# Performance work log

Hardware: AMD Instinct MI355X
Metric: run time of the kernel (lower is better)

The kernel has to match this reference:

```python
import jax, jax.numpy as jnp
import numpy as np
from jax import lax

B = 16           # graphs per batch
N_PER = 4096     # points per graph (equal-sized graphs)
C_IN = 32        # in_channels
RATIO = 0.25
MAX_NBR = 32     # max_num_neighbors in radius()


def _xavier(key, fan_in, fan_out):
    lim = np.sqrt(6.0 / (fan_in + fan_out)).astype(np.float32)
    return jax.random.uniform(key, (fan_in, fan_out), jnp.float32, -lim, lim)


def setup_inputs() -> dict:
    key = jax.random.key(0)
    ks = jax.random.split(key, 16)
    x = jax.random.normal(ks[0], (B * N_PER, C_IN), jnp.float32)
    pos = jax.random.uniform(ks[1], (B * N_PER, 3), jnp.float32) * 20.0
    batch = jnp.repeat(jnp.arange(B, dtype=jnp.int64), N_PER)
    p = {
        'x': x, 'pos': pos, 'batch': batch,
        'scaler_mean': jnp.zeros((1, C_IN), jnp.float32),
        'scaler_std': jnp.ones((1, C_IN), jnp.float32),
        # SA1: Linear(32+3,64) -> Sigmoid -> Linear(64,128)
        'sa1_w1': _xavier(ks[2], C_IN + 3, 64), 'sa1_b1': jnp.zeros((64,), jnp.float32),
        'sa1_w2': _xavier(ks[3], 64, 128),      'sa1_b2': jnp.zeros((128,), jnp.float32),
        # SA2: Linear(128+3,128) -> Sigmoid -> Linear(128,256)
        'sa2_w1': _xavier(ks[4], 128 + 3, 128), 'sa2_b1': jnp.zeros((128,), jnp.float32),
        'sa2_w2': _xavier(ks[5], 128, 256),     'sa2_b2': jnp.zeros((256,), jnp.float32),
        # Global SA: Linear(256+3,256) -> Sigmoid -> Linear(256,512)
        'g_w1': _xavier(ks[6], 256 + 3, 256),   'g_b1': jnp.zeros((256,), jnp.float32),
        'g_w2': _xavier(ks[7], 256, 512),       'g_b2': jnp.zeros((512,), jnp.float32),
        # fc: Linear(512,256) -> Sigmoid -> Linear(256,128)
        'fc_w1': _xavier(ks[8], 512, 256),      'fc_b1': jnp.zeros((256,), jnp.float32),
        'fc_w2': _xavier(ks[9], 256, 128),      'fc_b2': jnp.zeros((128,), jnp.float32),
    }
    return p


def _fps(pos, k):
    # Farthest point sampling, deterministic start at index 0. pos: [B, n, 3] -> idx [B, k]
    pos = lax.stop_gradient(pos)
    d0 = jnp.sum((pos - pos[:, :1, :]) ** 2, -1)  # [B, n] dist^2 to start point

    def step(mind, _):
        nxt = jnp.argmax(mind, axis=1)                                  # [B]
        p = jnp.take_along_axis(pos, nxt[:, None, None], axis=1)        # [B,1,3]
        mind = jnp.minimum(mind, jnp.sum((pos - p) ** 2, -1))
        return mind, nxt

    _, rest = lax.scan(step, d0, None, length=k - 1)                    # [k-1, B]
    start = jnp.zeros((1, pos.shape[0]), rest.dtype)
    return jnp.concatenate([start, rest], 0).T                          # [B, k]


def _gather_nbr(v, nbr):
    # v: [B, n, C], nbr: [B, k, MAX_NBR] -> [B, k, MAX_NBR, C]
    return jax.vmap(lambda vb, nb: vb[nb])(v, nbr)


def _sa_module(x, pos, w1, b1, w2, b2, ratio, r):
    # PointNetConv (max aggregation) over a radius graph from FPS centers.
    Bb, n, _ = x.shape
    k = int(n * ratio)
    idx = _fps(pos, k)                                                  # [B, k]
    pos_dst = jnp.take_along_axis(pos, idx[:, :, None], axis=1)         # [B, k, 3]
    d2 = jnp.sum((pos_dst[:, :, None, :] - pos[:, None, :, :]) ** 2, -1)  # [B,k,n]
    masked = jnp.where(d2 <= r * r, d2, jnp.inf)
    negv, nbr = lax.top_k(-masked, MAX_NBR)                             # nearest <=32 within radius
    valid = jnp.isfinite(negv)                                          # [B,k,32]
    x_j = _gather_nbr(x, nbr)                                           # [B,k,32,C]
    rel = _gather_nbr(pos, nbr) - pos_dst[:, :, None, :]                # pos_j - pos_i
    feat = jnp.concatenate([x_j, rel], axis=-1)
    msg = jax.nn.sigmoid(feat @ w1 + b1) @ w2 + b2                      # [B,k,32,2h]
    msg = jnp.where(valid[..., None], msg, -jnp.inf)
    agg = jnp.max(msg, axis=2)                                          # max aggregation
    agg = jnp.where(jnp.isfinite(agg), agg, 0.0)  # (self is always a neighbor, defensive)
    return jax.nn.relu(agg), pos_dst


def reference(x, pos, batch, scaler_mean, scaler_std,
              sa1_w1, sa1_b1, sa1_w2, sa1_b2,
              sa2_w1, sa2_b1, sa2_w2, sa2_b2,
              g_w1, g_b1, g_w2, g_b2,
              fc_w1, fc_b1, fc_w2, fc_b2):
    x = (x - scaler_mean) / scaler_std
    xb = x.reshape(B, N_PER, -1)      # batch is sorted with N_PER points per graph
    pb = pos.reshape(B, N_PER, 3)
    xb, pb = _sa_module(xb, pb, sa1_w1, sa1_b1, sa1_w2, sa1_b2, RATIO, 2.0)
    xb, pb = _sa_module(xb, pb, sa2_w1, sa2_b1, sa2_w2, sa2_b2, RATIO, 4.0)
    # GlobalSAModule: relu(nn(cat[x, pos])) then global max pool
    h = jnp.concatenate([xb, pb], axis=-1)
    h = jax.nn.relu(jax.nn.sigmoid(h @ g_w1 + g_b1) @ g_w2 + g_b2)      # [B, 256, 512]
    g = jnp.max(h, axis=1)                                              # [B, 512]
    out = jax.nn.sigmoid(g @ fc_w1 + fc_b1) @ fc_w2 + fc_b2
    return jax.nn.relu(out)                                             # last_act='relu'
```

## Files before the change

### kernel.cpp

```cpp
#include <hip/hip_runtime.h>
#include <hip/hip_bf16.h>
#include <math.h>

namespace {

constexpr int NB   = 16;
constexpr int N1   = 4096;
constexpr int K1   = 1024;
constexpr int K2   = 256;
constexpr int MAXN = 32;
constexpr int RCAP = 448;

__device__ __forceinline__ float sigmoidf_(float x) {
  return 1.0f / (1.0f + __expf(-x));
}

__device__ __forceinline__ float readlane_f(float v, int l) {
  return __int_as_float(__builtin_amdgcn_readlane(__float_as_int(v), l));
}


#define FPS_DPP_STEP(CTRL)                                                     \
  {                                                                            \
    const unsigned olo =                                                       \
        (unsigned)__builtin_amdgcn_update_dpp(0, (int)lo, (CTRL), 0xF, 0xF, true); \
    const unsigned ohi =                                                       \
        (unsigned)__builtin_amdgcn_update_dpp(0, (int)hi, (CTRL), 0xF, 0xF, true); \
    const unsigned long long o = ((unsigned long long)ohi << 32) | olo;        \
    const unsigned long long cur = ((unsigned long long)hi << 32) | lo;        \
    if (o > cur) { lo = olo; hi = ohi; }                                       \
  }

template<int NPT>
__device__ __forceinline__ void fps_level(
    const float* __restrict__ sx, const float* __restrict__ sy,
    const float* __restrict__ sz, int k,
    float* __restrict__ selx, float* __restrict__ sely,
    float* __restrict__ selz,
    unsigned long long (*red)[4]) {
  const int t = threadIdx.x;
  const int lane = t & 63, wave = t >> 6;
  float px[NPT], py[NPT], pz[NPT], mind[NPT];
  unsigned niv[NPT];
  const float c0x = sx[0], c0y = sy[0], c0z = sz[0];
  unsigned long long best = 0;
#pragma unroll
  for (int i = 0; i < NPT; i++) {
    const int p = i * 256 + t;
    niv[i] = ~(unsigned)p;
    px[i] = sx[p]; py[i] = sy[p]; pz[i] = sz[p];
    const float dx = px[i] - c0x, dy = py[i] - c0y, dz = pz[i] - c0z;
    const float d2 = dx * dx + dy * dy + dz * dz;
    mind[i] = d2;
    const unsigned long long cand =
        ((unsigned long long)__float_as_uint(d2) << 32) | niv[i];
    if (cand > best) best = cand;
  }
  if (t == 0) { selx[0] = c0x; sely[0] = c0y; selz[0] = c0z; }
  for (int it = 1; it < k; it++) {
    unsigned lo = (unsigned)best, hi = (unsigned)(best >> 32);
    FPS_DPP_STEP(0x111)
    FPS_DPP_STEP(0x112)
    FPS_DPP_STEP(0x114)
    FPS_DPP_STEP(0x118)
    FPS_DPP_STEP(0x142)
    FPS_DPP_STEP(0x143)
    const int par = it & 1;
    if (lane == 63) red[par][wave] = ((unsigned long long)hi << 32) | lo;
    __syncthreads();
    const unsigned long long w0 = red[par][0], w1 = red[par][1];
    const unsigned long long w2 = red[par][2], w3 = red[par][3];
    const unsigned long long m01 = w0 > w1 ? w0 : w1;
    const unsigned long long m23 = w2 > w3 ? w2 : w3;
    const unsigned long long win = m01 > m23 ? m01 : m23;
    const int p = (int)(~(unsigned)win);
    const float nx = sx[p], ny = sy[p], nz = sz[p];
    if (t == 0) { selx[it] = nx; sely[it] = ny; selz[it] = nz; }
    best = 0;
#pragma unroll
    for (int i = 0; i < NPT; i++) {
      const float dx = px[i] - nx, dy = py[i] - ny, dz = pz[i] - nz;
      const float d2 = dx * dx + dy * dy + dz * dz;
      const float m = fminf(mind[i], d2);
      mind[i] = m;
      const unsigned long long cand =
          ((unsigned long long)__float_as_uint(m) << 32) | niv[i];
      if (cand > best) best = cand;
    }
  }
}

#undef FPS_DPP_STEP

__global__ __launch_bounds__(256) void fps_l1_kernel(
    const float* __restrict__ pos,
    float* __restrict__ pxg, float* __restrict__ pyg, float* __restrict__ pzg,
    float* __restrict__ d1x, float* __restrict__ d1y, float* __restrict__ d1z,
    unsigned int* __restrict__ gout) {
  __shared__ float sx[N1], sy[N1], sz[N1];
  __shared__ float s2x[K1], s2y[K1], s2z[K1];
  __shared__ __align__(16) unsigned long long red[2][4];
  const int b = blockIdx.x;
  const int t = threadIdx.x;
  gout[b * 512 + t] = 0u;
  gout[b * 512 + t + 256] = 0u;
  const float* pb = pos + (size_t)b * N1 * 3;
  for (int p = t; p < N1; p += 256) {
    sx[p] = pb[p * 3 + 0]; sy[p] = pb[p * 3 + 1]; sz[p] = pb[p * 3 + 2];
  }
  __syncthreads();
  fps_level<N1 / 256>(sx, sy, sz, K1, s2x, s2y, s2z, red);
  __syncthreads();
  for (int p = t; p < N1; p += 256) {
    pxg[(size_t)b * N1 + p] = sx[p];
    pyg[(size_t)b * N1 + p] = sy[p];
    pzg[(size_t)b * N1 + p] = sz[p];
  }
  for (int i = t; i < K1; i += 256) {
    d1x[(size_t)b * K1 + i] = s2x[i];
    d1y[(size_t)b * K1 + i] = s2y[i];
    d1z[(size_t)b * K1 + i] = s2z[i];
  }
}

struct RadSmem {
  float candd[4][RCAP];
  int   candi[4][RCAP];
};

__device__ __forceinline__ void radius_body(
    const float* __restrict__ ptsx, const float* __restrict__ ptsy,
    const float* __restrict__ ptsz, int N,
    const float* __restrict__ cxs, const float* __restrict__ cys,
    const float* __restrict__ czs, int K, int CSTR, float r2,
    int* __restrict__ nbr, int* __restrict__ cnt_out, RadSmem& sm, int rb) {
  const int t = threadIdx.x;
  const int lane = t & 63, wave = t >> 6;
  const int bpg = K / 4;
  const int b = rb / bpg;
  const int ci = (rb % bpg) * 4 + wave;
  const size_t pbase = (size_t)b * N;
  const size_t cbase = (size_t)b * CSTR + ci;
  const float cx = cxs[cbase], cy = cys[cbase], cz = czs[cbase];
  int total = 0;
  for (int base = 0; base < N; base += 64) {
    const int p = base + lane;
    const float dx = ptsx[pbase + p] - cx;
    const float dy = ptsy[pbase + p] - cy;
    const float dz = ptsz[pbase + p] - cz;
    const float d2 = dx * dx + dy * dy + dz * dz;
    const bool pred = d2 <= r2;
    const unsigned long long m = __ballot(pred);
    if (pred) {
      const int slot = total + __popcll(m & ((1ull << lane) - 1ull));
      if (slot < RCAP) { sm.candd[wave][slot] = d2; sm.candi[wave][slot] = p; }
    }
    total += __popcll(m);
  }
  if (total > RCAP) total = RCAP;
  int* nbp = nbr + ((size_t)b * K + ci) * MAXN;
  if (total <= MAXN) {
    if (lane < total) nbp[lane] = sm.candi[wave][lane];
  } else {
    for (int jj = 0; jj < MAXN; jj++) {
      float bvd = INFINITY; int bvi = 0x7fffffff; int bslot = 0;
      for (int s = lane; s < total; s += 64) {
        const float d = sm.candd[wave][s];
        const int i = sm.candi[wave][s];
        if (d < bvd || (d == bvd && i < bvi)) { bvd = d; bvi = i; bslot = s; }
      }
#pragma unroll
      for (int off = 32; off; off >>= 1) {
        const float od = __shfl_xor(bvd, off);
        const int   oi = __shfl_xor(bvi, off);
        const int   os = __shfl_xor(bslot, off);
        if (od < bvd || (od == bvd && oi < bvi)) { bvd = od; bvi = oi; bslot = os; }
      }
      if (lane == 0) { nbp[jj] = bvi; sm.candd[wave][bslot] = INFINITY; }
    }
  }
  if (lane == 0) cnt_out[(size_t)b * K + ci] = (total < MAXN) ? total : MAXN;
}

__global__ __launch_bounds__(256) void rad12_kernel(
    const float* __restrict__ pxg, const float* __restrict__ pyg,
    const float* __restrict__ pzg,
    const float* __restrict__ d1x, const float* __restrict__ d1y,
    const float* __restrict__ d1z,
    int* __restrict__ nbr1, int* __restrict__ cnt1,
    int* __restrict__ nbr2, int* __restrict__ cnt2) {
  constexpr int NR1 = NB * K1 / 4;
  __shared__ __align__(16) RadSmem r;
  if (blockIdx.x < (unsigned)NR1) {
    radius_body(pxg, pyg, pzg, N1, d1x, d1y, d1z, K1, K1, 4.0f,
                nbr1, cnt1, r, blockIdx.x);
  } else {
    radius_body(d1x, d1y, d1z, K1, d1x, d1y, d1z, K2, K1, 16.0f,
                nbr2, cnt2, r, blockIdx.x - NR1);
  }
}

template<int CIN_T, int H, int COUT, bool SCALE>
__device__ __forceinline__ void sa_conv_body(
    const float* __restrict__ xin,
    const float* __restrict__ ptsx, const float* __restrict__ ptsy,
    const float* __restrict__ ptsz,
    const float* __restrict__ cxs, const float* __restrict__ cys,
    const float* __restrict__ czs,
    const int* __restrict__ nbr, const int* __restrict__ cnt,
    const float* __restrict__ w1, const float* __restrict__ b1,
    const float* __restrict__ w2, const float* __restrict__ b2,
    const float* __restrict__ smean, const float* __restrict__ sstd,
    int N, int K, int CSTR, float* __restrict__ xout,
    float* part , int bk) {
  constexpr int FIN  = CIN_T + 3;
  constexpr int KREG = (FIN + 63) / 64;
  constexpr int HREG = H / 64;
  constexpr int CREG = COUT / 64;
  constexpr int RPW  = MAXN / 4;
  const int t = threadIdx.x, lane = t & 63, wave = t >> 6;
  const int b = bk / K;
  const int V = cnt[bk];
  float m[CREG];
#pragma unroll
  for (int ck = 0; ck < CREG; ck++) m[ck] = -INFINITY;
  if (V > wave * RPW) {
    const int* nb = nbr + (size_t)bk * MAXN;
    const size_t crow = (size_t)b * CSTR + (bk - b * K);
    const float ctrx = cxs[crow];
    const float ctry = cys[crow];
    const float ctrz = czs[crow];
    float sm = 0.0f, sd = 1.0f;
    if (SCALE && lane < CIN_T) { sm = smean[lane]; sd = sstd[lane]; }
    float fr[RPW][KREG];
#pragma unroll
    for (int r = 0; r < RPW; r++) {
      const int j = wave * RPW + r;
      const int p = (j < V) ? nb[j] : nb[0];
#pragma unroll
      for (int k2 = 0; k2 < KREG; k2++) {
        const int f = k2 * 64 + lane;
        float v = 0.0f;
        if (f < CIN_T) {
          v = xin[((size_t)b * N + p) * CIN_T + f];
          if constexpr (SCALE) v = (v - sm) / sd;
        } else if (f < FIN) {
          const int d = f - CIN_T;
          const float pv = (d == 0 ? ptsx : (d == 1 ? ptsy : ptsz))[(size_t)b * N + p];
          v = pv - (d == 0 ? ctrx : (d == 1 ? ctry : ctrz));
        }
        fr[r][k2] = v;
      }
    }
    float hh[RPW][HREG];
    {
      float acc[RPW][HREG];
#pragma unroll
      for (int r = 0; r < RPW; r++)
#pragma unroll
        for (int q = 0; q < HREG; q++) acc[r][q] = 0.0f;
#pragma unroll
      for (int k2 = 0; k2 < KREG; k2++) {
        const int lim = (FIN - k2 * 64) < 64 ? (FIN - k2 * 64) : 64;
        for (int fl = 0; fl < lim; fl++) {
          const int f = k2 * 64 + fl;
          float wv[HREG];
          if constexpr (HREG == 1) {
            wv[0] = w1[(size_t)f * H + lane];
          } else {
            const float2 w = *reinterpret_cast<const float2*>(
                &w1[(size_t)f * H + lane * 2]);
            wv[0] = w.x; wv[1] = w.y;
          }
#pragma unroll
          for (int r = 0; r < RPW; r++) {
            const float s = readlane_f(fr[r][k2], fl);
#pragma unroll
            for (int q = 0; q < HREG; q++) acc[r][q] = fmaf(s, wv[q], acc[r][q]);
          }
        }
      }
#pragma unroll
      for (int q = 0; q < HREG; q++) {
        const float bb = b1[lane * HREG + q];
#pragma unroll
        for (int r = 0; r < RPW; r++) hh[r][q] = sigmoidf_(acc[r][q] + bb);
      }
    }
    float acc2[RPW][CREG];
#pragma unroll
    for (int r = 0; r < RPW; r++)
#pragma unroll
      for (int q = 0; q < CREG; q++) acc2[r][q] = 0.0f;
    for (int hl = 0; hl < 64; hl++) {
#pragma unroll
      for (int q1 = 0; q1 < HREG; q1++) {
        const int h = hl * HREG + q1;
        float wv[CREG];
        if constexpr (CREG == 2) {
          const float2 w = *reinterpret_cast<const float2*>(
              &w2[(size_t)h * COUT + lane * 2]);
          wv[0] = w.x; wv[1] = w.y;
        } else {
          const float4 w = *reinterpret_cast<const float4*>(
              &w2[(size_t)h * COUT + lane * 4]);
          wv[0] = w.x; wv[1] = w.y; wv[2] = w.z; wv[3] = w.w;
        }
#pragma unroll
        for (int r = 0; r < RPW; r++) {
          const float s = readlane_f(hh[r][q1], hl);
#pragma unroll
          for (int q = 0; q < CREG; q++) acc2[r][q] = fmaf(s, wv[q], acc2[r][q]);
        }
      }
    }
#pragma unroll
    for (int r = 0; r < RPW; r++) {
      if (wave * RPW + r < V) {
#pragma unroll
        for (int q = 0; q < CREG; q++) m[q] = fmaxf(m[q], acc2[r][q]);
      }
    }
  }
#pragma unroll
  for (int q = 0; q < CREG; q++) part[wave * COUT + lane * CREG + q] = m[q];
  __syncthreads();
  if (t < COUT) {
    const float mm = fmaxf(fmaxf(part[0 * COUT + t], part[1 * COUT + t]),
                           fmaxf(part[2 * COUT + t], part[3 * COUT + t]));
    const float o = mm + b2[t];
    xout[(size_t)bk * COUT + t] = o > 0.0f ? o : 0.0f;
  }
}

__global__ __launch_bounds__(256) void conv1_kernel(
    const float* __restrict__ x,
    const float* __restrict__ pxg, const float* __restrict__ pyg,
    const float* __restrict__ pzg,
    const float* __restrict__ d1x, const float* __restrict__ d1y,
    const float* __restrict__ d1z,
    const int* __restrict__ nbr1, const int* __restrict__ cnt1,
    const float* __restrict__ s1w1, const float* __restrict__ s1b1,
    const float* __restrict__ s1w2, const float* __restrict__ s1b2,
    const float* __restrict__ smean, const float* __restrict__ sstd,
    float* __restrict__ x1) {
  __shared__ __align__(16) float part[4 * 128];
  sa_conv_body<32, 64, 128, true>(x, pxg, pyg, pzg, d1x, d1y, d1z,
                                  nbr1, cnt1, s1w1, s1b1, s1w2, s1b2,
                                  smean, sstd, N1, K1, K1, x1, part,
                                  blockIdx.x);
}

__global__ __launch_bounds__(256) void conv2_kernel(
    const float* __restrict__ x1,
    const float* __restrict__ d1x, const float* __restrict__ d1y,
    const float* __restrict__ d1z,
    const int* __restrict__ nbr2, const int* __restrict__ cnt2,
    const float* __restrict__ s2w1, const float* __restrict__ s2b1,
    const float* __restrict__ s2w2, const float* __restrict__ s2b2,
    float* __restrict__ x2) {
  __shared__ __align__(16) float part[4 * 256];
  sa_conv_body<128, 128, 256, false>(x1, d1x, d1y, d1z, d1x, d1y, d1z,
                                     nbr2, cnt2, s2w1, s2b1, s2w2, s2b2,
                                     nullptr, nullptr, K1, K2, K1, x2, part,
                                     blockIdx.x);
}

__global__ __launch_bounds__(256) void global_sa_kernel(
    const float* __restrict__ x2,
    const float* __restrict__ d1x, const float* __restrict__ d1y,
    const float* __restrict__ d1z,
    const float* __restrict__ gw1, const float* __restrict__ gb1,
    const float* __restrict__ gw2, const float* __restrict__ gb2,
    unsigned int* __restrict__ gout) {
  __shared__ float fin[4][259];
  __shared__ float s[4][256];
  const int t = threadIdx.x;
  const int blk = blockIdx.x;
  const int b = blk / 64;
  const int p0 = (blk % 64) * 4;
  for (int item = t; item < 4 * 259; item += 256) {
    const int p = item / 259, f = item - p * 259;
    float v;
    if (f < 256) {
      v = x2[((size_t)b * 256 + p0 + p) * 256 + f];
    } else {
      const int d = f - 256;
      v = (d == 0 ? d1x : (d == 1 ? d1y : d1z))[(size_t)b * K1 + p0 + p];
    }
    fin[p][f] = v;
  }
  __syncthreads();
  float acc[4] = {0.f, 0.f, 0.f, 0.f};
  for (int f = 0; f < 259; f++) {
    const float w = gw1[f * 256 + t];
#pragma unroll
    for (int p = 0; p < 4; p++) acc[p] = fmaf(fin[p][f], w, acc[p]);
  }
  const float bb = gb1[t];
#pragma unroll
  for (int p = 0; p < 4; p++) s[p][t] = sigmoidf_(acc[p] + bb);
  __syncthreads();
  float a0[4] = {0.f, 0.f, 0.f, 0.f}, a1[4] = {0.f, 0.f, 0.f, 0.f};
  for (int h = 0; h < 256; h++) {
    const float w0 = gw2[h * 512 + t];
    const float w1v = gw2[h * 512 + t + 256];
#pragma unroll
    for (int p = 0; p < 4; p++) {
      a0[p] = fmaf(s[p][h], w0, a0[p]);
      a1[p] = fmaf(s[p][h], w1v, a1[p]);
    }
  }
  const float b0 = gb2[t], b1v = gb2[t + 256];
  float m0 = 0.0f, m1 = 0.0f;
#pragma unroll
  for (int p = 0; p < 4; p++) {
    m0 = fmaxf(m0, fmaxf(a0[p] + b0, 0.0f));
    m1 = fmaxf(m1, fmaxf(a1[p] + b1v, 0.0f));
  }
  atomicMax(&gout[b * 512 + t], __float_as_uint(m0));
  atomicMax(&gout[b * 512 + t + 256], __float_as_uint(m1));
}

__global__ __launch_bounds__(256) void fc_kernel(
    const unsigned int* __restrict__ g,
    const float* __restrict__ fw1, const float* __restrict__ fb1,
    const float* __restrict__ fw2, const float* __restrict__ fb2,
    float* __restrict__ out) {
  __shared__ float gv[512];
  __shared__ float s[256];
  const int b = blockIdx.x, t = threadIdx.x;
  gv[t] = __uint_as_float(g[b * 512 + t]);
  gv[t + 256] = __uint_as_float(g[b * 512 + t + 256]);
  __syncthreads();
  float acc = 0.0f;
  for (int h = 0; h < 512; h++) acc = fmaf(gv[h], fw1[h * 256 + t], acc);
  s[t] = sigmoidf_(acc + fb1[t]);
  __syncthreads();
  if (t < 128) {
    float a2 = 0.0f;
    for (int h = 0; h < 256; h++) a2 = fmaf(s[h], fw2[h * 128 + t], a2);
    const float o = a2 + fb2[t];
    out[b * 128 + t] = o > 0.0f ? o : 0.0f;
  }
}

}

extern "C" void kernel_launch(void* const* d_in, const int* in_sizes, int n_in,
                              void* d_out, int out_size, void* d_ws, size_t ws_size,
                              hipStream_t stream) {
  (void)in_sizes; (void)n_in; (void)out_size; (void)ws_size;
  const float* x     = (const float*)d_in[0];
  const float* pos   = (const float*)d_in[1];
  const float* smean = (const float*)d_in[3];
  const float* sstd  = (const float*)d_in[4];
  const float* s1w1  = (const float*)d_in[5];
  const float* s1b1  = (const float*)d_in[6];
  const float* s1w2  = (const float*)d_in[7];
  const float* s1b2  = (const float*)d_in[8];
  const float* s2w1  = (const float*)d_in[9];
  const float* s2b1  = (const float*)d_in[10];
  const float* s2w2  = (const float*)d_in[11];
  const float* s2b2  = (const float*)d_in[12];
  const float* gw1   = (const float*)d_in[13];
  const float* gb1   = (const float*)d_in[14];
  const float* gw2   = (const float*)d_in[15];
  const float* gb2   = (const float*)d_in[16];
  const float* fw1   = (const float*)d_in[17];
  const float* fb1   = (const float*)d_in[18];
  const float* fw2   = (const float*)d_in[19];
  const float* fb2   = (const float*)d_in[20];

  char* ws = (char*)d_ws;
  size_t off = 0;
  auto take = [&](size_t bytes) -> char* {
    char* p = ws + off;
    off = (off + bytes + 255) & ~(size_t)255;
    return p;
  };
  float* pxg         = (float*)take((size_t)NB * N1 * 4);
  float* pyg         = (float*)take((size_t)NB * N1 * 4);
  float* pzg         = (float*)take((size_t)NB * N1 * 4);
  float* d1x         = (float*)take((size_t)NB * K1 * 4);
  float* d1y         = (float*)take((size_t)NB * K1 * 4);
  float* d1z         = (float*)take((size_t)NB * K1 * 4);
  int*   nbr1        = (int*)take((size_t)NB * K1 * MAXN * 4);
  int*   cnt1        = (int*)take((size_t)NB * K1 * 4);
  float* x1          = (float*)take((size_t)NB * K1 * 128 * 4);
  int*   nbr2        = (int*)take((size_t)NB * K2 * MAXN * 4);
  int*   cnt2        = (int*)take((size_t)NB * K2 * 4);
  float* x2          = (float*)take((size_t)NB * K2 * 256 * 4);
  unsigned int* gbuf = (unsigned int*)take((size_t)NB * 512 * 4);

  hipLaunchKernelGGL(fps_l1_kernel, dim3(NB), dim3(256), 0, stream,
                     pos, pxg, pyg, pzg, d1x, d1y, d1z, gbuf);
  hipLaunchKernelGGL(rad12_kernel, dim3(NB * K1 / 4 + NB * K2 / 4), dim3(256), 0, stream,
                     pxg, pyg, pzg, d1x, d1y, d1z, nbr1, cnt1, nbr2, cnt2);
  hipLaunchKernelGGL(conv1_kernel, dim3(NB * K1), dim3(256), 0, stream,
                     x, pxg, pyg, pzg, d1x, d1y, d1z, nbr1, cnt1,
                     s1w1, s1b1, s1w2, s1b2, smean, sstd, x1);
  hipLaunchKernelGGL(conv2_kernel, dim3(NB * K2), dim3(256), 0, stream,
                     x1, d1x, d1y, d1z, nbr2, cnt2,
                     s2w1, s2b1, s2w2, s2b2, x2);
  hipLaunchKernelGGL(global_sa_kernel, dim3(NB * 64), dim3(256), 0, stream,
                     x2, d1x, d1y, d1z, gw1, gb1, gw2, gb2, gbuf);
  hipLaunchKernelGGL(fc_kernel, dim3(NB), dim3(256), 0, stream,
                     gbuf, fw1, fb1, fw2, fb2, (float*)d_out);
}
```

Baseline: 1.150 ms.

## Overlap FPS with radius and conv1 in a persistent cooperative kernel

Replaces the separate FPS, radius and conv1 launches with one cooperative persistent kernel. Sixteen blocks run farthest-point sampling and publish progress through release-stored flags every four samples. The remaining blocks take work items from an atomic counter, spin until their centers are ready, then run the radius search and conv1 for four centers, keeping neighbor lists in LDS. The second-level radius search is also fused into the conv2 kernel, removing the global neighbor buffers and two launches. The trade-offs are spin-wait overhead, relying on the cooperative launch to make all 256 blocks co-resident, and subtle memory-ordering assumptions on the position writes.

```diff
diff --git a/kernel.cpp b/kernel.cpp
--- a/kernel.cpp
+++ b/kernel.cpp
@@ -32,12 +32,11 @@
   }
 
 template<int NPT>
-__device__ __forceinline__ void fps_level(
+__device__ __forceinline__ void fps_run(
     const float* __restrict__ sx, const float* __restrict__ sy,
     const float* __restrict__ sz, int k,
-    float* __restrict__ selx, float* __restrict__ sely,
-    float* __restrict__ selz,
-    unsigned long long (*red)[4]) {
+    float* __restrict__ dgx, float* __restrict__ dgy, float* __restrict__ dgz,
+    int* readyp, unsigned long long (*red)[4]) {
   const int t = threadIdx.x;
   const int lane = t & 63, wave = t >> 6;
   float px[NPT], py[NPT], pz[NPT], mind[NPT];
@@ -56,7 +55,7 @@
         ((unsigned long long)__float_as_uint(d2) << 32) | niv[i];
     if (cand > best) best = cand;
   }
-  if (t == 0) { selx[0] = c0x; sely[0] = c0y; selz[0] = c0z; }
+  if (t == 0) { dgx[0] = c0x; dgy[0] = c0y; dgz[0] = c0z; }
   for (int it = 1; it < k; it++) {
     unsigned lo = (unsigned)best, hi = (unsigned)(best >> 32);
     FPS_DPP_STEP(0x111)
@@ -75,7 +74,12 @@
     const unsigned long long win = m01 > m23 ? m01 : m23;
     const int p = (int)(~(unsigned)win);
     const float nx = sx[p], ny = sy[p], nz = sz[p];
-    if (t == 0) { selx[it] = nx; sely[it] = ny; selz[it] = nz; }
+    if (t == 0) {
+      dgx[it] = nx; dgy[it] = ny; dgz[it] = nz;
+      if ((it & 3) == 3)
+        __hip_atomic_store(readyp, it + 1, __ATOMIC_RELEASE,
+                           __HIP_MEMORY_SCOPE_AGENT);
+    }
     best = 0;
 #pragma unroll
     for (int i = 0; i < NPT; i++) {
@@ -88,66 +92,28 @@
       if (cand > best) best = cand;
     }
   }
+  if (t == 0)
+    __hip_atomic_store(readyp, k, __ATOMIC_RELEASE, __HIP_MEMORY_SCOPE_AGENT);
 }
 
 #undef FPS_DPP_STEP
-
-__global__ __launch_bounds__(256) void fps_l1_kernel(
-    const float* __restrict__ pos,
-    float* __restrict__ pxg, float* __restrict__ pyg, float* __restrict__ pzg,
-    float* __restrict__ d1x, float* __restrict__ d1y, float* __restrict__ d1z,
-    unsigned int* __restrict__ gout) {
-  __shared__ float sx[N1], sy[N1], sz[N1];
-  __shared__ float s2x[K1], s2y[K1], s2z[K1];
-  __shared__ __align__(16) unsigned long long red[2][4];
-  const int b = blockIdx.x;
-  const int t = threadIdx.x;
-  gout[b * 512 + t] = 0u;
-  gout[b * 512 + t + 256] = 0u;
-  const float* pb = pos + (size_t)b * N1 * 3;
-  for (int p = t; p < N1; p += 256) {
-    sx[p] = pb[p * 3 + 0]; sy[p] = pb[p * 3 + 1]; sz[p] = pb[p * 3 + 2];
-  }
-  __syncthreads();
-  fps_level<N1 / 256>(sx, sy, sz, K1, s2x, s2y, s2z, red);
-  __syncthreads();
-  for (int p = t; p < N1; p += 256) {
-    pxg[(size_t)b * N1 + p] = sx[p];
-    pyg[(size_t)b * N1 + p] = sy[p];
-    pzg[(size_t)b * N1 + p] = sz[p];
-  }
-  for (int i = t; i < K1; i += 256) {
-    d1x[(size_t)b * K1 + i] = s2x[i];
-    d1y[(size_t)b * K1 + i] = s2y[i];
-    d1z[(size_t)b * K1 + i] = s2z[i];
-  }
-}
 
 struct RadSmem {
   float candd[4][RCAP];
   int   candi[4][RCAP];
 };
 
-__device__ __forceinline__ void radius_body(
-    const float* __restrict__ ptsx, const float* __restrict__ ptsy,
-    const float* __restrict__ ptsz, int N,
-    const float* __restrict__ cxs, const float* __restrict__ cys,
-    const float* __restrict__ czs, int K, int CSTR, float r2,
-    int* __restrict__ nbr, int* __restrict__ cnt_out, RadSmem& sm, int rb) {
-  const int t = threadIdx.x;
-  const int lane = t & 63, wave = t >> 6;
-  const int bpg = K / 4;
-  const int b = rb / bpg;
-  const int ci = (rb % bpg) * 4 + wave;
-  const size_t pbase = (size_t)b * N;
-  const size_t cbase = (size_t)b * CSTR + ci;
-  const float cx = cxs[cbase], cy = cys[cbase], cz = czs[cbase];
+__device__ __forceinline__ void radius_lds(
+    const float* __restrict__ px, const float* __restrict__ py,
+    const float* __restrict__ pz, int N,
+    float cx, float cy, float cz, float r2,
+    RadSmem& sm, int* nb, int* cntp, int wave, int lane) {
   int total = 0;
   for (int base = 0; base < N; base += 64) {
     const int p = base + lane;
-    const float dx = ptsx[pbase + p] - cx;
-    const float dy = ptsy[pbase + p] - cy;
-    const float dz = ptsz[pbase + p] - cz;
+    const float dx = px[p] - cx;
+    const float dy = py[p] - cy;
+    const float dz = pz[p] - cz;
     const float d2 = dx * dx + dy * dy + dz * dz;
     const bool pred = d2 <= r2;
     const unsigned long long m = __ballot(pred);
@@ -158,9 +124,8 @@
     total += __popcll(m);
   }
   if (total > RCAP) total = RCAP;
-  int* nbp = nbr + ((size_t)b * K + ci) * MAXN;
   if (total <= MAXN) {
-    if (lane < total) nbp[lane] = sm.candi[wave][lane];
+    if (lane < total) nb[lane] = sm.candi[wave][lane];
   } else {
     for (int jj = 0; jj < MAXN; jj++) {
       float bvd = INFINITY; int bvi = 0x7fffffff; int bslot = 0;
@@ -176,60 +141,33 @@
         const int   os = __shfl_xor(bslot, off);
         if (od < bvd || (od == bvd && oi < bvi)) { bvd = od; bvi = oi; bslot = os; }
       }
-      if (lane == 0) { nbp[jj] = bvi; sm.candd[wave][bslot] = INFINITY; }
-    }
-  }
-  if (lane == 0) cnt_out[(size_t)b * K + ci] = (total < MAXN) ? total : MAXN;
-}
-
-__global__ __launch_bounds__(256) void rad12_kernel(
-    const float* __restrict__ pxg, const float* __restrict__ pyg,
-    const float* __restrict__ pzg,
-    const float* __restrict__ d1x, const float* __restrict__ d1y,
-    const float* __restrict__ d1z,
-    int* __restrict__ nbr1, int* __restrict__ cnt1,
-    int* __restrict__ nbr2, int* __restrict__ cnt2) {
-  constexpr int NR1 = NB * K1 / 4;
-  __shared__ __align__(16) RadSmem r;
-  if (blockIdx.x < (unsigned)NR1) {
-    radius_body(pxg, pyg, pzg, N1, d1x, d1y, d1z, K1, K1, 4.0f,
-                nbr1, cnt1, r, blockIdx.x);
-  } else {
-    radius_body(d1x, d1y, d1z, K1, d1x, d1y, d1z, K2, K1, 16.0f,
-                nbr2, cnt2, r, blockIdx.x - NR1);
-  }
+      if (lane == 0) { nb[jj] = bvi; sm.candd[wave][bslot] = INFINITY; }
+    }
+  }
+  if (lane == 0) *cntp = (total < MAXN) ? total : MAXN;
 }
 
 template<int CIN_T, int H, int COUT, bool SCALE>
-__device__ __forceinline__ void sa_conv_body(
+__device__ __forceinline__ void conv_center(
     const float* __restrict__ xin,
     const float* __restrict__ ptsx, const float* __restrict__ ptsy,
     const float* __restrict__ ptsz,
-    const float* __restrict__ cxs, const float* __restrict__ cys,
-    const float* __restrict__ czs,
-    const int* __restrict__ nbr, const int* __restrict__ cnt,
+    float ctrx, float ctry, float ctrz,
+    const int* nb, int V,
     const float* __restrict__ w1, const float* __restrict__ b1,
     const float* __restrict__ w2, const float* __restrict__ b2,
     const float* __restrict__ smean, const float* __restrict__ sstd,
-    int N, int K, int CSTR, float* __restrict__ xout,
-    float* part , int bk) {
+    float* __restrict__ outrow, float* part ) {
   constexpr int FIN  = CIN_T + 3;
   constexpr int KREG = (FIN + 63) / 64;
   constexpr int HREG = H / 64;
   constexpr int CREG = COUT / 64;
   constexpr int RPW  = MAXN / 4;
   const int t = threadIdx.x, lane = t & 63, wave = t >> 6;
-  const int b = bk / K;
-  const int V = cnt[bk];
   float m[CREG];
 #pragma unroll
   for (int ck = 0; ck < CREG; ck++) m[ck] = -INFINITY;
   if (V > wave * RPW) {
-    const int* nb = nbr + (size_t)bk * MAXN;
-    const size_t crow = (size_t)b * CSTR + (bk - b * K);
-    const float ctrx = cxs[crow];
-    const float ctry = cys[crow];
-    const float ctrz = czs[crow];
     float sm = 0.0f, sd = 1.0f;
     if (SCALE && lane < CIN_T) { sm = smean[lane]; sd = sstd[lane]; }
     float fr[RPW][KREG];
@@ -242,11 +180,11 @@
         const int f = k2 * 64 + lane;
         float v = 0.0f;
         if (f < CIN_T) {
-          v = xin[((size_t)b * N + p) * CIN_T + f];
+          v = xin[(size_t)p * CIN_T + f];
           if constexpr (SCALE) v = (v - sm) / sd;
         } else if (f < FIN) {
           const int d = f - CIN_T;
-          const float pv = (d == 0 ? ptsx : (d == 1 ? ptsy : ptsz))[(size_t)b * N + p];
+          const float pv = (d == 0 ? ptsx : (d == 1 ? ptsy : ptsz))[p];
           v = pv - (d == 0 ? ctrx : (d == 1 ? ctry : ctrz));
         }
         fr[r][k2] = v;
@@ -329,41 +267,109 @@
     const float mm = fmaxf(fmaxf(part[0 * COUT + t], part[1 * COUT + t]),
                            fmaxf(part[2 * COUT + t], part[3 * COUT + t]));
     const float o = mm + b2[t];
-    xout[(size_t)bk * COUT + t] = o > 0.0f ? o : 0.0f;
-  }
-}
-
-__global__ __launch_bounds__(256) void conv1_kernel(
-    const float* __restrict__ x,
-    const float* __restrict__ pxg, const float* __restrict__ pyg,
-    const float* __restrict__ pzg,
-    const float* __restrict__ d1x, const float* __restrict__ d1y,
-    const float* __restrict__ d1z,
-    const int* __restrict__ nbr1, const int* __restrict__ cnt1,
+    outrow[t] = o > 0.0f ? o : 0.0f;
+  }
+}
+
+__global__ __launch_bounds__(256) void phase1_kernel(
+    const float* __restrict__ pos, const float* __restrict__ x,
+    const float* __restrict__ smean, const float* __restrict__ sstd,
     const float* __restrict__ s1w1, const float* __restrict__ s1b1,
     const float* __restrict__ s1w2, const float* __restrict__ s1b2,
-    const float* __restrict__ smean, const float* __restrict__ sstd,
-    float* __restrict__ x1) {
-  __shared__ __align__(16) float part[4 * 128];
-  sa_conv_body<32, 64, 128, true>(x, pxg, pyg, pzg, d1x, d1y, d1z,
-                                  nbr1, cnt1, s1w1, s1b1, s1w2, s1b2,
-                                  smean, sstd, N1, K1, K1, x1, part,
-                                  blockIdx.x);
-}
-
-__global__ __launch_bounds__(256) void conv2_kernel(
+    float* __restrict__ pxg, float* __restrict__ pyg, float* __restrict__ pzg,
+    float* __restrict__ d1x, float* __restrict__ d1y, float* __restrict__ d1z,
+    float* __restrict__ x1, unsigned int* __restrict__ gout,
+    int* __restrict__ ctrl) {
+  __shared__ __align__(16) char smem[49152];
+  __shared__ __align__(16) unsigned long long red[2][4];
+  __shared__ int s_item;
+  const int t = threadIdx.x, lane = t & 63, wave = t >> 6;
+  if (blockIdx.x < (unsigned)NB) {
+    const int b = blockIdx.x;
+    gout[b * 512 + t] = 0u;
+    gout[b * 512 + t + 256] = 0u;
+    float* sx = (float*)smem; float* sy = sx + N1; float* sz = sy + N1;
+    const float* pb = pos + (size_t)b * N1 * 3;
+    for (int p = t; p < N1; p += 256) {
+      sx[p] = pb[p * 3 + 0]; sy[p] = pb[p * 3 + 1]; sz[p] = pb[p * 3 + 2];
+    }
+    __syncthreads();
+    for (int p = t; p < N1; p += 256) {
+      pxg[(size_t)b * N1 + p] = sx[p];
+      pyg[(size_t)b * N1 + p] = sy[p];
+      pzg[(size_t)b * N1 + p] = sz[p];
+    }
+    fps_run<N1 / 256>(sx, sy, sz, K1,
+                      d1x + (size_t)b * K1, d1y + (size_t)b * K1,
+                      d1z + (size_t)b * K1, &ctrl[8 + b], red);
+    __syncthreads();
+  }
+  RadSmem& rs = *reinterpret_cast<RadSmem*>(smem);
+  int* nb_l = reinterpret_cast<int*>(smem + sizeof(RadSmem));
+  int* cnt_l = nb_l + 4 * MAXN;
+  float* part = reinterpret_cast<float*>(cnt_l + 4);
+  constexpr int NITEMS = NB * (K1 / 4);
+  for (;;) {
+    if (t == 0) s_item = atomicAdd(&ctrl[0], 1);
+    __syncthreads();
+    const int item = s_item;
+    __syncthreads();
+    if (item >= NITEMS) break;
+    const int b = item % NB, grp = item / NB;
+    if (t == 0) {
+      while (__hip_atomic_load(&ctrl[8 + b], __ATOMIC_ACQUIRE,
+                               __HIP_MEMORY_SCOPE_AGENT) < 4 * grp + 4)
+        __builtin_amdgcn_s_sleep(16);
+    }
+    __syncthreads();
+    const size_t pB = (size_t)b * N1, cB = (size_t)b * K1;
+    const int ci = 4 * grp + wave;
+    radius_lds(pxg + pB, pyg + pB, pzg + pB, N1,
+               d1x[cB + ci], d1y[cB + ci], d1z[cB + ci], 4.0f,
+               rs, nb_l + wave * MAXN, &cnt_l[wave], wave, lane);
+    __syncthreads();
+    for (int cc = 0; cc < 4; cc++) {
+      const int c2 = 4 * grp + cc;
+      conv_center<32, 64, 128, true>(
+          x + pB * 32, pxg + pB, pyg + pB, pzg + pB,
+          d1x[cB + c2], d1y[cB + c2], d1z[cB + c2],
+          nb_l + cc * MAXN, cnt_l[cc],
+          s1w1, s1b1, s1w2, s1b2, smean, sstd,
+          x1 + (cB + c2) * 128, part);
+      __syncthreads();
+    }
+  }
+}
+
+__global__ __launch_bounds__(256) void rad2conv2_kernel(
     const float* __restrict__ x1,
     const float* __restrict__ d1x, const float* __restrict__ d1y,
     const float* __restrict__ d1z,
-    const int* __restrict__ nbr2, const int* __restrict__ cnt2,
     const float* __restrict__ s2w1, const float* __restrict__ s2b1,
     const float* __restrict__ s2w2, const float* __restrict__ s2b2,
     float* __restrict__ x2) {
+  __shared__ __align__(16) RadSmem rs;
+  __shared__ int nb_l[4 * MAXN];
+  __shared__ int cnt_l[4];
   __shared__ __align__(16) float part[4 * 256];
-  sa_conv_body<128, 128, 256, false>(x1, d1x, d1y, d1z, d1x, d1y, d1z,
-                                     nbr2, cnt2, s2w1, s2b1, s2w2, s2b2,
-                                     nullptr, nullptr, K1, K2, K1, x2, part,
-                                     blockIdx.x);
+  const int t = threadIdx.x, lane = t & 63, wave = t >> 6;
+  const int b = blockIdx.x % NB, grp = blockIdx.x / NB;
+  const size_t cB = (size_t)b * K1;
+  const int ci = 4 * grp + wave;
+  radius_lds(d1x + cB, d1y + cB, d1z + cB, K1,
+             d1x[cB + ci], d1y[cB + ci], d1z[cB + ci], 16.0f,
+             rs, nb_l + wave * MAXN, &cnt_l[wave], wave, lane);
+  __syncthreads();
+  for (int cc = 0; cc < 4; cc++) {
+    const int c2 = 4 * grp + cc;
+    conv_center<128, 128, 256, false>(
+        x1 + cB * 128, d1x + cB, d1y + cB, d1z + cB,
+        d1x[cB + c2], d1y[cB + c2], d1z[cB + c2],
+        nb_l + cc * MAXN, cnt_l[cc],
+        s2w1, s2b1, s2w2, s2b2, nullptr, nullptr,
+        x2 + ((size_t)b * K2 + c2) * 256, part);
+    __syncthreads();
+  }
 }
 
 __global__ __launch_bounds__(256) void global_sa_kernel(
@@ -485,24 +491,25 @@
   float* d1x         = (float*)take((size_t)NB * K1 * 4);
   float* d1y         = (float*)take((size_t)NB * K1 * 4);
   float* d1z         = (float*)take((size_t)NB * K1 * 4);
-  int*   nbr1        = (int*)take((size_t)NB * K1 * MAXN * 4);
-  int*   cnt1        = (int*)take((size_t)NB * K1 * 4);
   float* x1          = (float*)take((size_t)NB * K1 * 128 * 4);
-  int*   nbr2        = (int*)take((size_t)NB * K2 * MAXN * 4);
-  int*   cnt2        = (int*)take((size_t)NB * K2 * 4);
   float* x2          = (float*)take((size_t)NB * K2 * 256 * 4);
   unsigned int* gbuf = (unsigned int*)take((size_t)NB * 512 * 4);
-
-  hipLaunchKernelGGL(fps_l1_kernel, dim3(NB), dim3(256), 0, stream,
-                     pos, pxg, pyg, pzg, d1x, d1y, d1z, gbuf);
-  hipLaunchKernelGGL(rad12_kernel, dim3(NB * K1 / 4 + NB * K2 / 4), dim3(256), 0, stream,
-                     pxg, pyg, pzg, d1x, d1y, d1z, nbr1, cnt1, nbr2, cnt2);
-  hipLaunchKernelGGL(conv1_kernel, dim3(NB * K1), dim3(256), 0, stream,
-                     x, pxg, pyg, pzg, d1x, d1y, d1z, nbr1, cnt1,
-                     s1w1, s1b1, s1w2, s1b2, smean, sstd, x1);
-  hipLaunchKernelGGL(conv2_kernel, dim3(NB * K2), dim3(256), 0, stream,
-                     x1, d1x, d1y, d1z, nbr2, cnt2,
-                     s2w1, s2b1, s2w2, s2b2, x2);
+  int* ctrl          = (int*)take(128);
+
+  hipMemsetAsync(ctrl, 0, 128, stream);
+
+  {
+    void* args[] = {
+        (void*)&pos, (void*)&x, (void*)&smean, (void*)&sstd,
+        (void*)&s1w1, (void*)&s1b1, (void*)&s1w2, (void*)&s1b2,
+        (void*)&pxg, (void*)&pyg, (void*)&pzg,
+        (void*)&d1x, (void*)&d1y, (void*)&d1z,
+        (void*)&x1, (void*)&gbuf, (void*)&ctrl};
+    hipLaunchCooperativeKernel((void*)phase1_kernel, dim3(256), dim3(256),
+                               args, 0, stream);
+  }
+  hipLaunchKernelGGL(rad2conv2_kernel, dim3(NB * K2 / 4), dim3(256), 0, stream,
+                     x1, d1x, d1y, d1z, s2w1, s2b1, s2w2, s2b2, x2);
   hipLaunchKernelGGL(global_sa_kernel, dim3(NB * 64), dim3(256), 0, stream,
                      x2, d1x, d1y, d1z, gw1, gb1, gw2, gb2, gbuf);
   hipLaunchKernelGGL(fc_kernel, dim3(NB), dim3(256), 0, stream,
```

After: 1.252 ms. 1.09x slower.
